# Kernel optimization log

Measured on AMD Instinct MI355X. Metric: run time of the kernel, lower is better.

## Reference

```python
import jax, jax.numpy as jnp
import numpy as np


def setup_inputs() -> dict:
    key = jax.random.key(0)
    ks = jax.random.split(key, 7)
    G, MC, B = 4, 100, 512
    IN, H, OUT = 456, 400, 10
    return {
        "x": jax.random.normal(ks[0], (B, IN), dtype=jnp.float32),
        "mu1": jax.random.normal(ks[1], (G, IN, H), dtype=jnp.float32),
        "sigma1": jax.random.normal(ks[2], (G, IN, H), dtype=jnp.float32),
        "mu3": jax.random.normal(ks[3], (G, H, OUT), dtype=jnp.float32),
        "sigma3": jax.random.normal(ks[4], (G, H, OUT), dtype=jnp.float32),
        "zeta1": jax.random.normal(ks[5], (G, MC, B, H), dtype=jnp.float32),
        "zeta3": jax.random.normal(ks[6], (G, MC, B, OUT), dtype=jnp.float32),
        "num": 3,
    }


def reference(x, mu1, sigma1, mu3, sigma3, zeta1, zeta3, num):
    # softplus(sigma)^2, the local-reparameterization variance term
    sp2 = lambda s: jnp.square(jnp.log1p(jnp.exp(s)))

    def one_net(m1, s1, m3, s3, z1, z3):
        # layer 1: local reparameterization trick (Kingma et al. 2015)
        g1 = x @ m1                               # [B, H]
        d1 = (x * x) @ sp2(s1)                    # [B, H]
        h = jax.nn.relu(g1 + jnp.sqrt(d1) * z1)   # [MC, B, H] via broadcast
        # layer 2
        g3 = jnp.einsum('mbh,ho->mbo', h, m3)     # [MC, B, OUT]
        d3 = jnp.einsum('mbh,ho->mbo', h * h, sp2(s3))
        o = jax.nn.relu(g3 + jnp.sqrt(d3) * z3)
        p = jax.nn.softmax(o, axis=-1)            # nn.Softmax over class dim
        return p.mean(axis=0)                     # average over MC samples

    G = num + 1
    outs = jax.vmap(one_net)(mu1[:G], sigma1[:G], mu3[:G], sigma3[:G],
                             zeta1[:G], zeta3[:G])  # [G, B, OUT]
    B = x.shape[0]
    # torch.cat((out_0, out_1, ...), dim=1)
    return jnp.transpose(outs, (1, 0, 2)).reshape(B, -1)
```

## Files before the change

kernel.cpp:

```cpp
#include <hip/hip_runtime.h>
#include <math.h>

#define GN  4
#define MCN 100
#define BN  512
#define INN 456
#define HN  400
#define ON  10

__device__ __forceinline__ float sp2f(float s) {
    float l = log1pf(__expf(-fabsf(s)));
    float r = fmaxf(s, 0.0f) + l;
    return r * r;
}

__global__ __launch_bounds__(256) void k_zero(float* __restrict__ out) {
    int i = blockIdx.x * 256 + threadIdx.x;
    if (i < BN * GN * ON) out[i] = 0.0f;
}

__global__ __launch_bounds__(256) void k_transpose(
    const float* __restrict__ x, float* __restrict__ xT, float* __restrict__ xxT) {
    __shared__ float tile[64][65];
    int it = blockIdx.x;
    int bt = blockIdx.y;
    int tx = threadIdx.x & 63;
    int ty = threadIdx.x >> 6;
    int i_in = it * 64 + tx;
    #pragma unroll
    for (int r = 0; r < 16; ++r) {
        int row = r * 4 + ty;
        int b = bt * 64 + row;
        tile[row][tx] = (i_in < INN) ? x[b * INN + i_in] : 0.0f;
    }
    __syncthreads();
    #pragma unroll
    for (int r = 0; r < 16; ++r) {
        int row = r * 4 + ty;
        int i = it * 64 + row;
        if (i < INN) {
            float v = tile[tx][row];
            xT[i * BN + bt * 64 + tx]  = v;
            xxT[i * BN + bt * 64 + tx] = v * v;
        }
    }
}

__global__ __launch_bounds__(256) void k_sp1(
    const float* __restrict__ sigma1, float* __restrict__ sp1) {
    int idx = blockIdx.x * 256 + threadIdx.x;
    const int n4 = GN * INN * HN / 4;
    if (idx < n4) {
        float4 s = ((const float4*)sigma1)[idx];
        float4 o;
        o.x = sp2f(s.x); o.y = sp2f(s.y); o.z = sp2f(s.z); o.w = sp2f(s.w);
        ((float4*)sp1)[idx] = o;
    }
}

__global__ __launch_bounds__(256) void k_layer1(
    const float* __restrict__ xT, const float* __restrict__ xxT,
    const float* __restrict__ mu1, const float* __restrict__ sp1,
    float* __restrict__ A, float* __restrict__ S) {
    int bt = blockIdx.x;
    int ht = blockIdx.y;
    int g  = blockIdx.z;
    int lane = threadIdx.x & 63;
    int wv   = threadIdx.x >> 6;
    int h = ht * 64 + lane;
    bool hv = h < HN;
    int hc = hv ? h : (HN - 1);
    int b0 = __builtin_amdgcn_readfirstlane(bt * 16 + wv * 4);
    const float* mp = mu1 + (size_t)g * INN * HN + hc;
    const float* pp = sp1 + (size_t)g * INN * HN + hc;
    float accA[4] = {0.f, 0.f, 0.f, 0.f};
    float accD[4] = {0.f, 0.f, 0.f, 0.f};
    #pragma unroll 4
    for (int k = 0; k < INN; ++k) {
        float a = mp[(size_t)k * HN];
        float p = pp[(size_t)k * HN];
        float4 xv  = *(const float4*)(xT  + k * BN + b0);
        float4 xxv = *(const float4*)(xxT + k * BN + b0);
        accA[0] = fmaf(a, xv.x,  accA[0]);
        accA[1] = fmaf(a, xv.y,  accA[1]);
        accA[2] = fmaf(a, xv.z,  accA[2]);
        accA[3] = fmaf(a, xv.w,  accA[3]);
        accD[0] = fmaf(p, xxv.x, accD[0]);
        accD[1] = fmaf(p, xxv.y, accD[1]);
        accD[2] = fmaf(p, xxv.z, accD[2]);
        accD[3] = fmaf(p, xxv.w, accD[3]);
    }
    if (hv) {
        #pragma unroll
        for (int j = 0; j < 4; ++j) {
            size_t o = ((size_t)g * BN + (b0 + j)) * HN + h;
            A[o] = accA[j];
            S[o] = sqrtf(accD[j]);
        }
    }
}

__global__ __launch_bounds__(256, 3) void k_layer2(
    const float* __restrict__ A, const float* __restrict__ S,
    const float* __restrict__ mu3, const float* __restrict__ sigma3,
    const float* __restrict__ zeta1, const float* __restrict__ zeta3,
    float* __restrict__ out) {
    int b  = blockIdx.x;
    int g  = blockIdx.y;
    int mb = blockIdx.z * 64;

    __shared__ float as_s[2 * HN];
    __shared__ float wv_s[HN * 20];
    __shared__ float outsh[16][ON];

    int t = threadIdx.x;

    for (int i = t; i < HN; i += 256) {
        size_t src = ((size_t)g * BN + b) * HN + i;
        as_s[2 * i]     = A[src];
        as_s[2 * i + 1] = S[src];
    }
    for (int i = t; i < HN * ON; i += 256) {
        int h = i / ON, o = i % ON;
        int wslot = (o < 4) ? o       : (o < 8) ? (4 + o) : (8 + o);
        int vslot = (o < 4) ? (4 + o) : (o < 8) ? (8 + o) : (10 + o);
        size_t src = (size_t)(g * HN + h) * ON + o;
        wv_s[h * 20 + wslot] = mu3[src];
        wv_s[h * 20 + vslot] = sp2f(sigma3[src]);
    }
    __syncthreads();

    int rg = t >> 4;
    int kc = t & 15;

    float accg[4][ON], accd[4][ON];
    #pragma unroll
    for (int i = 0; i < 4; ++i)
        #pragma unroll
        for (int o = 0; o < ON; ++o) { accg[i][o] = 0.0f; accd[i][o] = 0.0f; }

    const float* zp[4];
    #pragma unroll
    for (int i = 0; i < 4; ++i) {
        int m = mb + rg + 16 * i;
        int mcl = m < MCN ? m : (MCN - 1);
        zp[i] = zeta1 + ((size_t)(g * MCN + mcl) * BN + b) * HN + kc;
    }

    float zc[4];
    #pragma unroll
    for (int i = 0; i < 4; ++i) zc[i] = zp[i][0];

    #pragma unroll 1
    for (int j = 0; j < 25; ++j) {
        float zn[4];
        if (j < 24) {
            #pragma unroll
            for (int i = 0; i < 4; ++i) zn[i] = zp[i][16 * (j + 1)];
        } else {
            #pragma unroll
            for (int i = 0; i < 4; ++i) zn[i] = 0.0f;
        }
        int k = kc + 16 * j;
        float2 as = *(const float2*)(as_s + 2 * k);
        const float* wr = wv_s + k * 20;
        float4 w03 = *(const float4*)(wr);
        float4 v03 = *(const float4*)(wr + 4);
        float4 w47 = *(const float4*)(wr + 8);
        float4 v47 = *(const float4*)(wr + 12);
        float4 t4  = *(const float4*)(wr + 16);
        #pragma unroll
        for (int i = 0; i < 4; ++i) {
            float hval = fmaxf(0.0f, fmaf(as.y, zc[i], as.x));
            float h2 = hval * hval;
            accg[i][0] = fmaf(hval, w03.x, accg[i][0]);
            accg[i][1] = fmaf(hval, w03.y, accg[i][1]);
            accg[i][2] = fmaf(hval, w03.z, accg[i][2]);
            accg[i][3] = fmaf(hval, w03.w, accg[i][3]);
            accg[i][4] = fmaf(hval, w47.x, accg[i][4]);
            accg[i][5] = fmaf(hval, w47.y, accg[i][5]);
            accg[i][6] = fmaf(hval, w47.z, accg[i][6]);
            accg[i][7] = fmaf(hval, w47.w, accg[i][7]);
            accg[i][8] = fmaf(hval, t4.x,  accg[i][8]);
            accg[i][9] = fmaf(hval, t4.y,  accg[i][9]);
            accd[i][0] = fmaf(h2, v03.x, accd[i][0]);
            accd[i][1] = fmaf(h2, v03.y, accd[i][1]);
            accd[i][2] = fmaf(h2, v03.z, accd[i][2]);
            accd[i][3] = fmaf(h2, v03.w, accd[i][3]);
            accd[i][4] = fmaf(h2, v47.x, accd[i][4]);
            accd[i][5] = fmaf(h2, v47.y, accd[i][5]);
            accd[i][6] = fmaf(h2, v47.z, accd[i][6]);
            accd[i][7] = fmaf(h2, v47.w, accd[i][7]);
            accd[i][8] = fmaf(h2, t4.z,  accd[i][8]);
            accd[i][9] = fmaf(h2, t4.w,  accd[i][9]);
        }
        #pragma unroll
        for (int i = 0; i < 4; ++i) zc[i] = zn[i];
    }

    #pragma unroll
    for (int i = 0; i < 4; ++i) {
        #pragma unroll
        for (int o = 0; o < ON; ++o) {
            float vg = accg[i][o], vd = accd[i][o];
            vg += __shfl_xor(vg, 1);  vd += __shfl_xor(vd, 1);
            vg += __shfl_xor(vg, 2);  vd += __shfl_xor(vd, 2);
            vg += __shfl_xor(vg, 4);  vd += __shfl_xor(vd, 4);
            vg += __shfl_xor(vg, 8);  vd += __shfl_xor(vd, 8);
            accg[i][o] = vg; accd[i][o] = vd;
        }
    }

    if (kc == 0) {
        float psum[ON];
        #pragma unroll
        for (int o = 0; o < ON; ++o) psum[o] = 0.0f;
        #pragma unroll
        for (int i = 0; i < 4; ++i) {
            int m = mb + rg + 16 * i;
            if (m < MCN) {
                const float* z3p = zeta3 + ((size_t)(g * MCN + m) * BN + b) * ON;
                float ov[ON];
                float mx = 0.0f;
                #pragma unroll
                for (int o = 0; o < ON; ++o) {
                    float v = fmaf(sqrtf(accd[i][o]), z3p[o], accg[i][o]);
                    v = fmaxf(v, 0.0f);
                    ov[o] = v;
                    mx = fmaxf(mx, v);
                }
                float se = 0.0f;
                #pragma unroll
                for (int o = 0; o < ON; ++o) { float e = __expf(ov[o] - mx); ov[o] = e; se += e; }
                float r = 1.0f / se;
                #pragma unroll
                for (int o = 0; o < ON; ++o) psum[o] = fmaf(ov[o], r, psum[o]);
            }
        }
        #pragma unroll
        for (int o = 0; o < ON; ++o) outsh[rg][o] = psum[o];
    }
    __syncthreads();
    if (t < ON) {
        float s = 0.0f;
        #pragma unroll
        for (int r = 0; r < 16; ++r) s += outsh[r][t];
        atomicAdd(&out[b * (GN * ON) + g * ON + t], s * (1.0f / MCN));
    }
}

extern "C" void kernel_launch(void* const* d_in, const int* in_sizes, int n_in,
                              void* d_out, int out_size, void* d_ws, size_t ws_size,
                              hipStream_t stream) {
    const float* x      = (const float*)d_in[0];
    const float* mu1    = (const float*)d_in[1];
    const float* sigma1 = (const float*)d_in[2];
    const float* mu3    = (const float*)d_in[3];
    const float* sigma3 = (const float*)d_in[4];
    const float* zeta1  = (const float*)d_in[5];
    const float* zeta3  = (const float*)d_in[6];

    float* ws  = (float*)d_ws;
    float* xT  = ws;
    float* xxT = xT  + INN * BN;
    float* sp1 = xxT + INN * BN;
    float* A   = sp1 + GN * INN * HN;
    float* S   = A   + GN * BN * HN;
    float* out = (float*)d_out;

    k_zero<<<dim3((BN * GN * ON + 255) / 256), 256, 0, stream>>>(out);
    k_transpose<<<dim3(8, 8), 256, 0, stream>>>(x, xT, xxT);
    k_sp1<<<dim3((GN * INN * HN / 4 + 255) / 256), 256, 0, stream>>>(sigma1, sp1);
    k_layer1<<<dim3(32, 7, GN), 256, 0, stream>>>(xT, xxT, mu1, sp1, A, S);
    k_layer2<<<dim3(BN, GN, 2), 256, 0, stream>>>(A, S, mu3, sigma3, zeta1, zeta3, out);
}
```

Before: 666.2 us.

## Split layer2 mean/variance accumulation across two thread halves and trim MC tail

Layer 2 now runs 512-thread blocks: one half accumulates the mean projection (h·mu3), the other the variance projection (h²·sp2(sigma3)). Each thread holds half as many accumulators, which lowers register pressure and should allow higher occupancy. The variance results are exchanged through shared memory before the softmax. The MC dimension is split into two templated launches, TM=4 for the first 64 samples and TM=3 for the rest, so fewer clamped duplicate rows are computed; the cost is that each half reloads zeta1 and recomputes h. Layer1 also gets a launch-bounds hint, a larger unroll, and no longer uses readfirstlane.

```diff
diff --git a/kernel.cpp b/kernel.cpp
--- a/kernel.cpp
+++ b/kernel.cpp
@@ -58,7 +58,7 @@
     }
 }
 
-__global__ __launch_bounds__(256) void k_layer1(
+__global__ __launch_bounds__(256, 4) void k_layer1(
     const float* __restrict__ xT, const float* __restrict__ xxT,
     const float* __restrict__ mu1, const float* __restrict__ sp1,
     float* __restrict__ A, float* __restrict__ S) {
@@ -70,12 +70,12 @@
     int h = ht * 64 + lane;
     bool hv = h < HN;
     int hc = hv ? h : (HN - 1);
-    int b0 = __builtin_amdgcn_readfirstlane(bt * 16 + wv * 4);
+    int b0 = bt * 16 + wv * 4;
     const float* mp = mu1 + (size_t)g * INN * HN + hc;
     const float* pp = sp1 + (size_t)g * INN * HN + hc;
     float accA[4] = {0.f, 0.f, 0.f, 0.f};
     float accD[4] = {0.f, 0.f, 0.f, 0.f};
-    #pragma unroll 4
+    #pragma unroll 8
     for (int k = 0; k < INN; ++k) {
         float a = mp[(size_t)k * HN];
         float p = pp[(size_t)k * HN];
@@ -100,123 +100,128 @@
     }
 }
 
-__global__ __launch_bounds__(256, 3) void k_layer2(
+template <int TM, bool SQ>
+__device__ __forceinline__ void l2_loop(
+    const float* __restrict__ as_s, const float* __restrict__ wb,
+    const float* const (&zp)[TM], int kc, float (&acc)[TM][ON]) {
+    float zc[TM];
+    #pragma unroll
+    for (int i = 0; i < TM; ++i) zc[i] = zp[i][0];
+    #pragma unroll 1
+    for (int j = 0; j < 25; ++j) {
+        float zn[TM];
+        if (j < 24) {
+            #pragma unroll
+            for (int i = 0; i < TM; ++i) zn[i] = zp[i][16 * (j + 1)];
+        } else {
+            #pragma unroll
+            for (int i = 0; i < TM; ++i) zn[i] = 0.0f;
+        }
+        int k = kc + 16 * j;
+        float2 as = *(const float2*)(as_s + 2 * k);
+        const float* wr = wb + k * 12;
+        float4 wa = *(const float4*)(wr);
+        float4 wv = *(const float4*)(wr + 4);
+        float2 wc = *(const float2*)(wr + 8);
+        #pragma unroll
+        for (int i = 0; i < TM; ++i) {
+            float hv = fmaxf(0.0f, fmaf(as.y, zc[i], as.x));
+            float e = SQ ? hv * hv : hv;
+            acc[i][0] = fmaf(e, wa.x, acc[i][0]);
+            acc[i][1] = fmaf(e, wa.y, acc[i][1]);
+            acc[i][2] = fmaf(e, wa.z, acc[i][2]);
+            acc[i][3] = fmaf(e, wa.w, acc[i][3]);
+            acc[i][4] = fmaf(e, wv.x, acc[i][4]);
+            acc[i][5] = fmaf(e, wv.y, acc[i][5]);
+            acc[i][6] = fmaf(e, wv.z, acc[i][6]);
+            acc[i][7] = fmaf(e, wv.w, acc[i][7]);
+            acc[i][8] = fmaf(e, wc.x, acc[i][8]);
+            acc[i][9] = fmaf(e, wc.y, acc[i][9]);
+        }
+        #pragma unroll
+        for (int i = 0; i < TM; ++i) zc[i] = zn[i];
+    }
+}
+
+template <int TM>
+__global__ __launch_bounds__(512, 4) void k_layer2(
+    int mb,
     const float* __restrict__ A, const float* __restrict__ S,
     const float* __restrict__ mu3, const float* __restrict__ sigma3,
     const float* __restrict__ zeta1, const float* __restrict__ zeta3,
     float* __restrict__ out) {
-    int b  = blockIdx.x;
-    int g  = blockIdx.y;
-    int mb = blockIdx.z * 64;
+    int b = blockIdx.x;
+    int g = blockIdx.y;
 
     __shared__ float as_s[2 * HN];
-    __shared__ float wv_s[HN * 20];
+    __shared__ float w_s[HN * 12];
+    __shared__ float v_s[HN * 12];
+    __shared__ float d3x[16][TM][ON];
     __shared__ float outsh[16][ON];
 
     int t = threadIdx.x;
 
-    for (int i = t; i < HN; i += 256) {
+    for (int i = t; i < HN; i += 512) {
         size_t src = ((size_t)g * BN + b) * HN + i;
         as_s[2 * i]     = A[src];
         as_s[2 * i + 1] = S[src];
     }
-    for (int i = t; i < HN * ON; i += 256) {
-        int h = i / ON, o = i % ON;
-        int wslot = (o < 4) ? o       : (o < 8) ? (4 + o) : (8 + o);
-        int vslot = (o < 4) ? (4 + o) : (o < 8) ? (8 + o) : (10 + o);
-        size_t src = (size_t)(g * HN + h) * ON + o;
-        wv_s[h * 20 + wslot] = mu3[src];
-        wv_s[h * 20 + vslot] = sp2f(sigma3[src]);
-    }
-    __syncthreads();
-
-    int rg = t >> 4;
-    int kc = t & 15;
-
-    float accg[4][ON], accd[4][ON];
-    #pragma unroll
-    for (int i = 0; i < 4; ++i)
-        #pragma unroll
-        for (int o = 0; o < ON; ++o) { accg[i][o] = 0.0f; accd[i][o] = 0.0f; }
-
-    const float* zp[4];
-    #pragma unroll
-    for (int i = 0; i < 4; ++i) {
+    for (int i = t; i < HN * ON; i += 512) {
+        int h = i / 10, o = i - h * 10;
+        size_t src = (size_t)g * HN * ON + i;
+        w_s[h * 12 + o] = mu3[src];
+        v_s[h * 12 + o] = sp2f(sigma3[src]);
+    }
+    __syncthreads();
+
+    int og = t >> 8;
+    int th = t & 255;
+    int rg = th >> 4;
+    int kc = th & 15;
+
+    float acc[TM][ON];
+    #pragma unroll
+    for (int i = 0; i < TM; ++i)
+        #pragma unroll
+        for (int o = 0; o < ON; ++o) acc[i][o] = 0.0f;
+
+    const float* zp[TM];
+    #pragma unroll
+    for (int i = 0; i < TM; ++i) {
         int m = mb + rg + 16 * i;
         int mcl = m < MCN ? m : (MCN - 1);
         zp[i] = zeta1 + ((size_t)(g * MCN + mcl) * BN + b) * HN + kc;
     }
 
-    float zc[4];
-    #pragma unroll
-    for (int i = 0; i < 4; ++i) zc[i] = zp[i][0];
-
-    #pragma unroll 1
-    for (int j = 0; j < 25; ++j) {
-        float zn[4];
-        if (j < 24) {
+    if (og == 0) l2_loop<TM, false>(as_s, w_s, zp, kc, acc);
+    else         l2_loop<TM, true >(as_s, v_s, zp, kc, acc);
+
+    #pragma unroll
+    for (int i = 0; i < TM; ++i)
+        #pragma unroll
+        for (int o = 0; o < ON; ++o) {
+            float v = acc[i][o];
+            v += __shfl_xor(v, 1);
+            v += __shfl_xor(v, 2);
+            v += __shfl_xor(v, 4);
+            v += __shfl_xor(v, 8);
+            acc[i][o] = v;
+        }
+
+    if (og == 1 && kc == 0) {
+        #pragma unroll
+        for (int i = 0; i < TM; ++i)
             #pragma unroll
-            for (int i = 0; i < 4; ++i) zn[i] = zp[i][16 * (j + 1)];
-        } else {
-            #pragma unroll
-            for (int i = 0; i < 4; ++i) zn[i] = 0.0f;
-        }
-        int k = kc + 16 * j;
-        float2 as = *(const float2*)(as_s + 2 * k);
-        const float* wr = wv_s + k * 20;
-        float4 w03 = *(const float4*)(wr);
-        float4 v03 = *(const float4*)(wr + 4);
-        float4 w47 = *(const float4*)(wr + 8);
-        float4 v47 = *(const float4*)(wr + 12);
-        float4 t4  = *(const float4*)(wr + 16);
-        #pragma unroll
-        for (int i = 0; i < 4; ++i) {
-            float hval = fmaxf(0.0f, fmaf(as.y, zc[i], as.x));
-            float h2 = hval * hval;
-            accg[i][0] = fmaf(hval, w03.x, accg[i][0]);
-            accg[i][1] = fmaf(hval, w03.y, accg[i][1]);
-            accg[i][2] = fmaf(hval, w03.z, accg[i][2]);
-            accg[i][3] = fmaf(hval, w03.w, accg[i][3]);
-            accg[i][4] = fmaf(hval, w47.x, accg[i][4]);
-            accg[i][5] = fmaf(hval, w47.y, accg[i][5]);
-            accg[i][6] = fmaf(hval, w47.z, accg[i][6]);
-            accg[i][7] = fmaf(hval, w47.w, accg[i][7]);
-            accg[i][8] = fmaf(hval, t4.x,  accg[i][8]);
-            accg[i][9] = fmaf(hval, t4.y,  accg[i][9]);
-            accd[i][0] = fmaf(h2, v03.x, accd[i][0]);
-            accd[i][1] = fmaf(h2, v03.y, accd[i][1]);
-            accd[i][2] = fmaf(h2, v03.z, accd[i][2]);
-            accd[i][3] = fmaf(h2, v03.w, accd[i][3]);
-            accd[i][4] = fmaf(h2, v47.x, accd[i][4]);
-            accd[i][5] = fmaf(h2, v47.y, accd[i][5]);
-            accd[i][6] = fmaf(h2, v47.z, accd[i][6]);
-            accd[i][7] = fmaf(h2, v47.w, accd[i][7]);
-            accd[i][8] = fmaf(h2, t4.z,  accd[i][8]);
-            accd[i][9] = fmaf(h2, t4.w,  accd[i][9]);
-        }
-        #pragma unroll
-        for (int i = 0; i < 4; ++i) zc[i] = zn[i];
-    }
-
-    #pragma unroll
-    for (int i = 0; i < 4; ++i) {
-        #pragma unroll
-        for (int o = 0; o < ON; ++o) {
-            float vg = accg[i][o], vd = accd[i][o];
-            vg += __shfl_xor(vg, 1);  vd += __shfl_xor(vd, 1);
-            vg += __shfl_xor(vg, 2);  vd += __shfl_xor(vd, 2);
-            vg += __shfl_xor(vg, 4);  vd += __shfl_xor(vd, 4);
-            vg += __shfl_xor(vg, 8);  vd += __shfl_xor(vd, 8);
-            accg[i][o] = vg; accd[i][o] = vd;
-        }
-    }
-
-    if (kc == 0) {
+            for (int o = 0; o < ON; ++o) d3x[rg][i][o] = sqrtf(acc[i][o]);
+    }
+    __syncthreads();
+
+    if (og == 0 && kc == 0) {
         float psum[ON];
         #pragma unroll
         for (int o = 0; o < ON; ++o) psum[o] = 0.0f;
         #pragma unroll
-        for (int i = 0; i < 4; ++i) {
+        for (int i = 0; i < TM; ++i) {
             int m = mb + rg + 16 * i;
             if (m < MCN) {
                 const float* z3p = zeta3 + ((size_t)(g * MCN + m) * BN + b) * ON;
@@ -224,7 +229,7 @@
                 float mx = 0.0f;
                 #pragma unroll
                 for (int o = 0; o < ON; ++o) {
-                    float v = fmaf(sqrtf(accd[i][o]), z3p[o], accg[i][o]);
+                    float v = fmaf(d3x[rg][i][o], z3p[o], acc[i][o]);
                     v = fmaxf(v, 0.0f);
                     ov[o] = v;
                     mx = fmaxf(mx, v);
@@ -272,5 +277,6 @@
     k_transpose<<<dim3(8, 8), 256, 0, stream>>>(x, xT, xxT);
     k_sp1<<<dim3((GN * INN * HN / 4 + 255) / 256), 256, 0, stream>>>(sigma1, sp1);
     k_layer1<<<dim3(32, 7, GN), 256, 0, stream>>>(xT, xxT, mu1, sp1, A, S);
-    k_layer2<<<dim3(BN, GN, 2), 256, 0, stream>>>(A, S, mu3, sigma3, zeta1, zeta3, out);
-}
+    k_layer2<4><<<dim3(BN, GN), 512, 0, stream>>>(0,  A, S, mu3, sigma3, zeta1, zeta3, out);
+    k_layer2<3><<<dim3(BN, GN), 512, 0, stream>>>(64, A, S, mu3, sigma3, zeta1, zeta3, out);
+}
```

Measured after the change: 719.6 us. +8.0%, slower.
